# Kernel tuning notes

Measured on AMD Instinct MI355X. Metric: run time of the kernel, lower is better.

The kernel has to match this reference:

```python
import jax, jax.numpy as jnp
from jax import lax
import numpy as np

B, C, H, Wd = 32, 128, 56, 56
FILTERS = 128
KH = KW = 3
T_MIN_PREV = 0.0  # module defaults (set_params never called)
T_MIN = 0.0
T_MAX = 1.0


def setup_inputs() -> dict:
    key = jax.random.key(0)
    k1, k2 = jax.random.split(key)
    tj = jax.random.uniform(k1, (B, C, H, Wd), dtype=jnp.float32)          # spike times
    W = jax.random.normal(k2, (C * KH * KW, FILTERS), dtype=jnp.float32) * 0.02  # kernel.view(-1, filters)
    D_i = jnp.zeros((9, FILTERS), dtype=jnp.float32)                        # intrinsic delays (only row 0 used)
    return {"tj": tj, "W": W, "D_i": D_i}


def reference(tj, W, D_i):
    # 'same' padding with value t_min, then unfold + (tj - t_min) @ W is
    # exactly a zero-padded conv on (tj - t_min): the pad entries become 0.
    x = tj - T_MIN                                   # [B,C,H,W]
    # Unfold orders patch rows as (C, kh, kw); build the equivalent OIHW kernel.
    kernel = jnp.transpose(W.reshape(C, KH, KW, FILTERS), (3, 0, 1, 2))  # [F,C,KH,KW]
    y = lax.conv_general_dilated(
        x, kernel, window_strides=(1, 1), padding="SAME",
        dimension_numbers=("NCHW", "OIHW", "NCHW"))    # [B,F,H,W]
    threshold = T_MAX - T_MIN - D_i[0]                 # [F]
    ti = y + threshold[None, :, None, None] + T_MIN
    ti = jnp.minimum(ti, T_MAX)                        # torch.where(ti < t_max, ti, t_max)
    return jnp.transpose(ti, (0, 2, 3, 1))             # [B,H,W,F], matches ti.view(b,H,W,filters)
```

## Files before the change

### kernel.cpp

```cpp
#include <hip/hip_runtime.h>


#define BZ 32
#define CC 128
#define HH 56
#define WWD 56
#define HWP 3136
#define FF 128
#define PH 58
#define PW 58
#define QC 32
#define PATCH_G 2320
#define PATCH_BYTES 40960
#define BQ_OFF 81920
#define BQ_BYTES 8192
#define LDS_TOTAL 98304
#define NSTEP 36

typedef __attribute__((ext_vector_type(8))) __bf16 bf16x8;
typedef __attribute__((ext_vector_type(4))) float f32x4;
typedef __attribute__((ext_vector_type(8))) unsigned short us8;
typedef __attribute__((ext_vector_type(4))) float flt4;

__device__ __forceinline__ unsigned short f2bf(float f) {
  unsigned int u = __float_as_uint(f);
  unsigned int r = (u + 0x7FFFu + ((u >> 16) & 1u)) >> 16;
  return (unsigned short)r;
}

#define GLOAD_LDS16(g, l)                                                              \
  __builtin_amdgcn_global_load_lds((const __attribute__((address_space(1))) void*)(g), \
                                   (__attribute__((address_space(3))) void*)(l), 16, 0, 0)

__global__ void prep_w_kernel(const float* __restrict__ W, unsigned short* __restrict__ Wt) {
  int idx = blockIdx.x * 256 + threadIdx.x;
  if (idx >= 4 * 9 * 512) return;
  int qr = idx >> 9;
  int gp = idx & 511;
  int g = gp ^ ((gp >> 3) & 7);
  int q = qr / 9, r = qr - q * 9;
  int f = g >> 2, kg = g & 3;
  us8 v;
#pragma unroll
  for (int j = 0; j < 8; ++j) {
    int c = q * QC + kg * 8 + j;
    v[j] = f2bf(W[(c * 9 + r) * FF + f]);
  }
  *reinterpret_cast<us8*>(Wt + (size_t)idx * 8) = v;
}

__global__ __launch_bounds__(256) void prep_x_kernel(const float* __restrict__ x,
                                                     unsigned short* __restrict__ xp) {
  const int blk = blockIdx.x;
  const int b = blk / PH;
  const int ph = blk - b * PH;
  const int tid = threadIdx.x;
  unsigned short* dst = xp + (size_t)(b * PH + ph) * PW * CC;

  if (ph == 0 || ph == PH - 1) {
    us8 z;
#pragma unroll
    for (int k = 0; k < 8; ++k) z[k] = 0;
    for (int i = tid; i < PW * CC / 8; i += 256) reinterpret_cast<us8*>(dst)[i] = z;
    return;
  }

  __shared__ float sm[CC][57];
  const int h = ph - 1;
  {
    const int c = tid >> 1;
    const int half = tid & 1;
    const float* src = x + ((size_t)(b * CC + c)) * HWP + h * WWD + half * 28;
#pragma unroll
    for (int k = 0; k < 7; ++k) {
      flt4 v = *reinterpret_cast<const flt4*>(src + k * 4);
      sm[c][half * 28 + k * 4 + 0] = v[0];
      sm[c][half * 28 + k * 4 + 1] = v[1];
      sm[c][half * 28 + k * 4 + 2] = v[2];
      sm[c][half * 28 + k * 4 + 3] = v[3];
    }
  }
  __syncthreads();
  for (int i = tid; i < PW * 16; i += 256) {
    const int ww = i >> 4;
    const int cg = i & 15;
    us8 v;
    if (ww == 0 || ww == PW - 1) {
#pragma unroll
      for (int k = 0; k < 8; ++k) v[k] = 0;
    } else {
      const int w = ww - 1;
#pragma unroll
      for (int k = 0; k < 8; ++k) v[k] = f2bf(sm[cg * 8 + k][w]);
    }
    reinterpret_cast<us8*>(dst)[i] = v;
  }
}

struct Ctx {
  const unsigned short* xp;
  const unsigned short* Wt;
  int tid;
  int srcA[5];
  int gbase[7];
  int bOffB[4];
  f32x4 acc[7][4];
};

template <int S>
__device__ __forceinline__ void step(Ctx& c, unsigned char* lds) {
  constexpr int q = S / 9, r = S - q * 9;
  constexpr int dh = r / 3 - 1, dw = r - (r / 3) * 3 - 1;
  constexpr int tapoff = dh * 232 + dw * 4;
  constexpr bool issueA = (r < 5) && (q < 3);
  constexpr bool issueB = (S < NSTEP - 1);
  constexpr int nIssue = (issueA ? 1 : 0) + (issueB ? 1 : 0);

  if constexpr (issueA) {
    const unsigned short* src = c.xp + c.srcA[r] + (q + 1) * QC;
    unsigned char* dst = lds + ((q + 1) & 1) * PATCH_BYTES + (size_t)(r * 512 + c.tid) * 16;
    GLOAD_LDS16(src, dst);
  }
  if constexpr (issueB) {
    const unsigned short* src = c.Wt + (size_t)(S + 1) * 4096 + c.tid * 8;
    unsigned char* dst = lds + BQ_OFF + ((S + 1) & 1) * BQ_BYTES + (size_t)c.tid * 16;
    GLOAD_LDS16(src, dst);
  }
  asm volatile("s_waitcnt vmcnt(%0)" ::"n"(nIssue));
  __builtin_amdgcn_s_barrier();
  __builtin_amdgcn_sched_barrier(0);

  const unsigned char* pa = lds + (q & 1) * PATCH_BYTES;
  const unsigned char* pb = lds + BQ_OFF + (S & 1) * BQ_BYTES;
  bf16x8 af[7], bf[4];
#pragma unroll
  for (int i = 0; i < 7; ++i) {
    int g = c.gbase[i] + tapoff;
    int ga = (g ^ ((g >> 3) & 7)) << 4;
    af[i] = *reinterpret_cast<const bf16x8*>(pa + ga);
  }
#pragma unroll
  for (int j = 0; j < 4; ++j)
    bf[j] = *reinterpret_cast<const bf16x8*>(pb + c.bOffB[j]);

  __builtin_amdgcn_s_setprio(1);
#pragma unroll
  for (int i = 0; i < 7; ++i)
#pragma unroll
    for (int j = 0; j < 4; ++j)
      c.acc[i][j] = __builtin_amdgcn_mfma_f32_16x16x32_bf16(af[i], bf[j], c.acc[i][j], 0, 0, 0);
  __builtin_amdgcn_s_setprio(0);
  __builtin_amdgcn_sched_barrier(0);
  __builtin_amdgcn_s_barrier();
}

template <int S>
__device__ __forceinline__ void do_steps(Ctx& c, unsigned char* lds) {
  step<S>(c, lds);
  if constexpr (S + 1 < NSTEP) do_steps<S + 1>(c, lds);
}

__global__ __launch_bounds__(512, 2) void spiking_conv_main(
    const unsigned short* __restrict__ xp, const unsigned short* __restrict__ Wt,
    const float* __restrict__ Di, float* __restrict__ out) {
  extern __shared__ unsigned char lds[];

  const int bid = blockIdx.x;
  const int wg = (bid & 7) * 28 + (bid >> 3);
  const int b = wg / 7;
  const int ht = wg - b * 7;
  const int h0 = ht * 8;

  Ctx c;
  c.xp = xp;
  c.Wt = Wt;
  const int tid = threadIdx.x;
  c.tid = tid;
  const int lane = tid & 63, wv = tid >> 6;
  const int wr = wv >> 1, wc = wv & 1;
  const int frow = lane & 15, kg = lane >> 4;

#pragma unroll
  for (int k = 0; k < 5; ++k) {
    int gp = k * 512 + tid;
    int g = gp ^ ((gp >> 3) & 7);
    int ph = g / 232;
    int rem = g - ph * 232;
    int pw = rem >> 2;
    int kg2 = rem & 3;
    int e = ((b * PH + h0 + ph) * PW + pw) * CC + kg2 * 8;
    c.srcA[k] = (gp < PATCH_G) ? e : 0;
  }
#pragma unroll
  for (int i = 0; i < 7; ++i) {
    int t = 16 * i + frow;
    int hl = (t >= 56) ? 1 : 0;
    int wl = t - 56 * hl;
    c.gbase[i] = ((2 * wr + hl + 1) * 58 + (wl + 1)) * 4 + kg;
  }
#pragma unroll
  for (int j = 0; j < 4; ++j) {
    int gB = (wc * 64 + 16 * j + frow) * 4 + kg;
    c.bOffB[j] = (gB ^ ((gB >> 3) & 7)) << 4;
  }
  const f32x4 zero = {0.0f, 0.0f, 0.0f, 0.0f};
#pragma unroll
  for (int i = 0; i < 7; ++i)
#pragma unroll
    for (int j = 0; j < 4; ++j) c.acc[i][j] = zero;

#pragma unroll
  for (int k = 0; k < 5; ++k)
    GLOAD_LDS16(xp + c.srcA[k], lds + (size_t)(k * 512 + tid) * 16);
  GLOAD_LDS16(Wt + tid * 8, lds + BQ_OFF + (size_t)tid * 16);
  asm volatile("s_waitcnt vmcnt(0)");
  __builtin_amdgcn_s_barrier();
  __builtin_amdgcn_sched_barrier(0);

  do_steps<0>(c, lds);

#pragma unroll
  for (int j = 0; j < 4; ++j) {
    const int col = wc * 64 + 16 * j + frow;
    const float thr = 1.0f - Di[col];
#pragma unroll
    for (int i = 0; i < 7; ++i) {
      const int bt = 16 * i + kg * 4;
      const int hl = (bt >= 56) ? 1 : 0;
      const int wl0 = bt - 56 * hl;
      const int orow = h0 + 2 * wr + hl;
      const size_t obase = ((size_t)b * HWP + (size_t)orow * WWD + wl0) * FF + col;
#pragma unroll
      for (int qq = 0; qq < 4; ++qq) {
        float v = c.acc[i][j][qq] + thr;
        out[obase + (size_t)qq * FF] = fminf(v, 1.0f);
      }
    }
  }
}

__global__ __launch_bounds__(256) void spiking_conv_fallback(
    const float* __restrict__ x, const float* __restrict__ Wf,
    const float* __restrict__ Di, float* __restrict__ out) {
  __shared__ unsigned short Asm2[128][32];
  __shared__ unsigned short Bsm2[128][32];
  const int tid = threadIdx.x;
  const int m0 = blockIdx.x * 128;
  const int mi = tid & 127;
  const int half = tid >> 7;
  const int m = m0 + mi;
  const int bimg = m / HWP;
  const int p = m - bimg * HWP;
  const int h = p / WWD;
  const int w = p - h * WWD;
  const int baseA = (bimg * CC) * HWP + h * WWD + w;
  const int lane = tid & 63;
  const int wid = tid >> 6;
  const int wr = wid >> 1;
  const int wc = wid & 1;
  const int frow = lane & 15;
  const int kg = lane >> 4;
  f32x4 acc[4][4];
  const f32x4 zero = {0.0f, 0.0f, 0.0f, 0.0f};
#pragma unroll
  for (int i = 0; i < 4; ++i)
#pragma unroll
    for (int j = 0; j < 4; ++j) acc[i][j] = zero;
  for (int r = 0; r < 9; ++r) {
    const int dh = r / 3 - 1;
    const int dw = r - (r / 3) * 3 - 1;
    const int hh = h + dh;
    const int ww2 = w + dw;
    const bool valid = ((unsigned)hh < (unsigned)HH) && ((unsigned)ww2 < (unsigned)WWD);
    const int aoff2 = baseA + dh * WWD + dw + half * 16 * HWP;
    for (int c0 = 0; c0 < CC; c0 += 32) {
      __syncthreads();
      {
        const float* src = x + aoff2 + c0 * HWP;
        us8 v0, v1;
#pragma unroll
        for (int i = 0; i < 8; ++i) {
          float f0 = valid ? src[i * HWP] : 0.0f;
          float f1 = valid ? src[(i + 8) * HWP] : 0.0f;
          v0[i] = f2bf(f0);
          v1[i] = f2bf(f1);
        }
        *reinterpret_cast<us8*>(&Asm2[mi][half * 16]) = v0;
        *reinterpret_cast<us8*>(&Asm2[mi][half * 16 + 8]) = v1;
      }
      {
        us8 v0, v1;
#pragma unroll
        for (int i = 0; i < 8; ++i) {
          int cc2 = c0 + half * 16 + i;
          v0[i] = f2bf(Wf[(cc2 * 9 + r) * FF + mi]);
          v1[i] = f2bf(Wf[((cc2 + 8) * 9 + r) * FF + mi]);
        }
        *reinterpret_cast<us8*>(&Bsm2[mi][half * 16]) = v0;
        *reinterpret_cast<us8*>(&Bsm2[mi][half * 16 + 8]) = v1;
      }
      __syncthreads();
      bf16x8 af[4], bfr[4];
#pragma unroll
      for (int i = 0; i < 4; ++i)
        af[i] = *reinterpret_cast<const bf16x8*>(&Asm2[wr * 64 + i * 16 + frow][kg * 8]);
#pragma unroll
      for (int j = 0; j < 4; ++j)
        bfr[j] = *reinterpret_cast<const bf16x8*>(&Bsm2[wc * 64 + j * 16 + frow][kg * 8]);
#pragma unroll
      for (int i = 0; i < 4; ++i)
#pragma unroll
        for (int j = 0; j < 4; ++j)
          acc[i][j] = __builtin_amdgcn_mfma_f32_16x16x32_bf16(af[i], bfr[j], acc[i][j], 0, 0, 0);
    }
  }
#pragma unroll
  for (int j = 0; j < 4; ++j) {
    const int col = wc * 64 + j * 16 + frow;
    const float thr = 1.0f - Di[col];
#pragma unroll
    for (int i = 0; i < 4; ++i) {
      const int rbase = m0 + wr * 64 + i * 16 + kg * 4;
#pragma unroll
      for (int qq = 0; qq < 4; ++qq) {
        float v = acc[i][j][qq] + thr;
        out[(size_t)(rbase + qq) * FF + col] = fminf(v, 1.0f);
      }
    }
  }
}

extern "C" void kernel_launch(void* const* d_in, const int* in_sizes, int n_in,
                              void* d_out, int out_size, void* d_ws, size_t ws_size,
                              hipStream_t stream) {
  const float* tj = (const float*)d_in[0];
  const float* W = (const float*)d_in[1];
  const float* Di = (const float*)d_in[2];
  float* out = (float*)d_out;

  const size_t wt_bytes = (size_t)4 * 9 * 512 * 16;
  const size_t xp_bytes = (size_t)BZ * PH * PW * CC * 2;
  unsigned short* Wt = (unsigned short*)d_ws;
  unsigned short* xp = (unsigned short*)((char*)d_ws + wt_bytes);

  bool fast = (ws_size >= wt_bytes + xp_bytes);
  if (fast) {
    prep_w_kernel<<<72, 256, 0, stream>>>(W, Wt);
    prep_x_kernel<<<BZ * PH, 256, 0, stream>>>(tj, xp);
    spiking_conv_main<<<224, 512, LDS_TOTAL, stream>>>(xp, Wt, Di, out);
    if (hipGetLastError() != hipSuccess) fast = false;
  }
  if (!fast) {
    spiking_conv_fallback<<<100352 / 128, 256, 0, stream>>>(tj, W, Di, out);
  }
}
```

Measured before the change: 58.40 us.

## Halve conv workgroup tile, triple-buffer weights, drop LDS swizzle

The main conv kernel now runs 448 workgroups of 256 threads, each covering 4 output rows instead of 8. This gives better CU coverage on a 256-CU part and lowers LDS use per block. Weight slices are triple-buffered and prefetched two steps ahead, with a vmcnt count that tracks outstanding loads across steps, and the initial full wait is removed. The XOR swizzle on the LDS A and B layouts is dropped, which simplifies addressing but may bring back bank conflicts.

```diff
diff --git a/kernel.cpp b/kernel.cpp
--- a/kernel.cpp
+++ b/kernel.cpp
@@ -9,13 +9,12 @@
 #define FF 128
 #define PH 58
 #define PW 58
-#define QC 32
-#define PATCH_G 2320
-#define PATCH_BYTES 40960
-#define BQ_OFF 81920
-#define BQ_BYTES 8192
-#define LDS_TOTAL 98304
 #define NSTEP 36
+#define AB_BYTES 24576
+#define A_GRAN_REAL 1392
+#define BOFF 49152
+#define BB_BYTES 8192
+#define LDS_TOTAL 73728
 
 typedef __attribute__((ext_vector_type(8))) __bf16 bf16x8;
 typedef __attribute__((ext_vector_type(4))) float f32x4;
@@ -34,16 +33,15 @@
 
 __global__ void prep_w_kernel(const float* __restrict__ W, unsigned short* __restrict__ Wt) {
   int idx = blockIdx.x * 256 + threadIdx.x;
-  if (idx >= 4 * 9 * 512) return;
+  if (idx >= NSTEP * 512) return;
   int qr = idx >> 9;
-  int gp = idx & 511;
-  int g = gp ^ ((gp >> 3) & 7);
+  int g = idx & 511;
   int q = qr / 9, r = qr - q * 9;
   int f = g >> 2, kg = g & 3;
   us8 v;
 #pragma unroll
   for (int j = 0; j < 8; ++j) {
-    int c = q * QC + kg * 8 + j;
+    int c = q * 32 + kg * 8 + j;
     v[j] = f2bf(W[(c * 9 + r) * FF + f]);
   }
   *reinterpret_cast<us8*>(Wt + (size_t)idx * 8) = v;
@@ -101,7 +99,7 @@
   const unsigned short* xp;
   const unsigned short* Wt;
   int tid;
-  int srcA[5];
+  int srcA[6];
   int gbase[7];
   int bOffB[4];
   f32x4 acc[7][4];
@@ -111,34 +109,36 @@
 __device__ __forceinline__ void step(Ctx& c, unsigned char* lds) {
   constexpr int q = S / 9, r = S - q * 9;
   constexpr int dh = r / 3 - 1, dw = r - (r / 3) * 3 - 1;
-  constexpr int tapoff = dh * 232 + dw * 4;
-  constexpr bool issueA = (r < 5) && (q < 3);
-  constexpr bool issueB = (S < NSTEP - 1);
-  constexpr int nIssue = (issueA ? 1 : 0) + (issueB ? 1 : 0);
+  constexpr int tapoff = (dh * PW + dw) * 4;
+  constexpr bool issueA = (q < 3) && (r < 6);
+  constexpr bool issueB = (S <= NSTEP - 3);
+  constexpr int aS = issueA ? 1 : 0;
+  constexpr int bS = issueB ? 2 : 0;
+  constexpr int aP = (S == 0) ? 0 : ((((S - 1) / 9) < 3 && ((S - 1) % 9) < 6) ? 1 : 0);
+  constexpr int bP = (S == 0) ? 2 : (((S - 1) <= NSTEP - 3) ? 2 : 0);
+  constexpr int nOut = aS + bS + aP + bP;
 
   if constexpr (issueA) {
-    const unsigned short* src = c.xp + c.srcA[r] + (q + 1) * QC;
-    unsigned char* dst = lds + ((q + 1) & 1) * PATCH_BYTES + (size_t)(r * 512 + c.tid) * 16;
+    const unsigned short* src = c.xp + c.srcA[r] + (q + 1) * 32;
+    unsigned char* dst = lds + ((q + 1) & 1) * AB_BYTES + (size_t)(r * 256 + c.tid) * 16;
     GLOAD_LDS16(src, dst);
   }
   if constexpr (issueB) {
-    const unsigned short* src = c.Wt + (size_t)(S + 1) * 4096 + c.tid * 8;
-    unsigned char* dst = lds + BQ_OFF + ((S + 1) & 1) * BQ_BYTES + (size_t)c.tid * 16;
+    const unsigned short* src = c.Wt + (size_t)(S + 2) * 4096 + c.tid * 8;
+    unsigned char* dst = lds + BOFF + ((S + 2) % 3) * BB_BYTES + (size_t)c.tid * 16;
     GLOAD_LDS16(src, dst);
-  }
-  asm volatile("s_waitcnt vmcnt(%0)" ::"n"(nIssue));
+    GLOAD_LDS16(src + 2048, dst + 4096);
+  }
+  asm volatile("s_waitcnt vmcnt(%0)" ::"n"(nOut));
   __builtin_amdgcn_s_barrier();
   __builtin_amdgcn_sched_barrier(0);
 
-  const unsigned char* pa = lds + (q & 1) * PATCH_BYTES;
-  const unsigned char* pb = lds + BQ_OFF + (S & 1) * BQ_BYTES;
+  const unsigned char* pa = lds + (q & 1) * AB_BYTES;
+  const unsigned char* pb = lds + BOFF + (S % 3) * BB_BYTES;
   bf16x8 af[7], bf[4];
 #pragma unroll
-  for (int i = 0; i < 7; ++i) {
-    int g = c.gbase[i] + tapoff;
-    int ga = (g ^ ((g >> 3) & 7)) << 4;
-    af[i] = *reinterpret_cast<const bf16x8*>(pa + ga);
-  }
+  for (int i = 0; i < 7; ++i)
+    af[i] = *reinterpret_cast<const bf16x8*>(pa + ((c.gbase[i] + tapoff) << 4));
 #pragma unroll
   for (int j = 0; j < 4; ++j)
     bf[j] = *reinterpret_cast<const bf16x8*>(pb + c.bOffB[j]);
@@ -160,16 +160,16 @@
   if constexpr (S + 1 < NSTEP) do_steps<S + 1>(c, lds);
 }
 
-__global__ __launch_bounds__(512, 2) void spiking_conv_main(
+__global__ __launch_bounds__(256, 2) void spiking_conv_main(
     const unsigned short* __restrict__ xp, const unsigned short* __restrict__ Wt,
     const float* __restrict__ Di, float* __restrict__ out) {
   extern __shared__ unsigned char lds[];
 
   const int bid = blockIdx.x;
-  const int wg = (bid & 7) * 28 + (bid >> 3);
-  const int b = wg / 7;
-  const int ht = wg - b * 7;
-  const int h0 = ht * 8;
+  const int wg = (bid & 7) * 56 + (bid >> 3);
+  const int b = wg / 14;
+  const int rg = wg - b * 14;
+  const int h0 = rg * 4;
 
   Ctx c;
   c.xp = xp;
@@ -181,28 +181,26 @@
   const int frow = lane & 15, kg = lane >> 4;
 
 #pragma unroll
-  for (int k = 0; k < 5; ++k) {
-    int gp = k * 512 + tid;
-    int g = gp ^ ((gp >> 3) & 7);
-    int ph = g / 232;
-    int rem = g - ph * 232;
-    int pw = rem >> 2;
+  for (int k = 0; k < 6; ++k) {
+    int g = k * 256 + tid;
+    if (g >= A_GRAN_REAL) g = 0;
+    int prow = g / 232;
+    int rem = g - prow * 232;
+    int px = rem >> 2;
     int kg2 = rem & 3;
-    int e = ((b * PH + h0 + ph) * PW + pw) * CC + kg2 * 8;
-    c.srcA[k] = (gp < PATCH_G) ? e : 0;
+    c.srcA[k] = ((b * PH + h0 + prow) * PW + px) * CC + kg2 * 8;
   }
 #pragma unroll
   for (int i = 0; i < 7; ++i) {
     int t = 16 * i + frow;
-    int hl = (t >= 56) ? 1 : 0;
-    int wl = t - 56 * hl;
-    c.gbase[i] = ((2 * wr + hl + 1) * 58 + (wl + 1)) * 4 + kg;
-  }
-#pragma unroll
-  for (int j = 0; j < 4; ++j) {
-    int gB = (wc * 64 + 16 * j + frow) * 4 + kg;
-    c.bOffB[j] = (gB ^ ((gB >> 3) & 7)) << 4;
-  }
+    int rowb = (t >= 56) ? 1 : 0;
+    int col = t - 56 * rowb;
+    c.gbase[i] = ((2 * wr + rowb + 1) * PW + (col + 1)) * 4 + kg;
+  }
+#pragma unroll
+  for (int j = 0; j < 4; ++j)
+    c.bOffB[j] = ((wc * 64 + 16 * j + frow) * 4 + kg) << 4;
+
   const f32x4 zero = {0.0f, 0.0f, 0.0f, 0.0f};
 #pragma unroll
   for (int i = 0; i < 7; ++i)
@@ -210,12 +208,12 @@
     for (int j = 0; j < 4; ++j) c.acc[i][j] = zero;
 
 #pragma unroll
-  for (int k = 0; k < 5; ++k)
-    GLOAD_LDS16(xp + c.srcA[k], lds + (size_t)(k * 512 + tid) * 16);
-  GLOAD_LDS16(Wt + tid * 8, lds + BQ_OFF + (size_t)tid * 16);
-  asm volatile("s_waitcnt vmcnt(0)");
-  __builtin_amdgcn_s_barrier();
-  __builtin_amdgcn_sched_barrier(0);
+  for (int k = 0; k < 6; ++k)
+    GLOAD_LDS16(xp + c.srcA[k], lds + (size_t)(k * 256 + tid) * 16);
+  GLOAD_LDS16(Wt + tid * 8, lds + BOFF + (size_t)tid * 16);
+  GLOAD_LDS16(Wt + 2048 + tid * 8, lds + BOFF + 4096 + (size_t)tid * 16);
+  GLOAD_LDS16(Wt + 4096 + tid * 8, lds + BOFF + BB_BYTES + (size_t)tid * 16);
+  GLOAD_LDS16(Wt + 6144 + tid * 8, lds + BOFF + BB_BYTES + 4096 + (size_t)tid * 16);
 
   do_steps<0>(c, lds);
 
@@ -226,9 +224,9 @@
 #pragma unroll
     for (int i = 0; i < 7; ++i) {
       const int bt = 16 * i + kg * 4;
-      const int hl = (bt >= 56) ? 1 : 0;
-      const int wl0 = bt - 56 * hl;
-      const int orow = h0 + 2 * wr + hl;
+      const int rowb = (bt >= 56) ? 1 : 0;
+      const int wl0 = bt - 56 * rowb;
+      const int orow = h0 + 2 * wr + rowb;
       const size_t obase = ((size_t)b * HWP + (size_t)orow * WWD + wl0) * FF + col;
 #pragma unroll
       for (int qq = 0; qq < 4; ++qq) {
@@ -338,7 +336,7 @@
   const float* Di = (const float*)d_in[2];
   float* out = (float*)d_out;
 
-  const size_t wt_bytes = (size_t)4 * 9 * 512 * 16;
+  const size_t wt_bytes = (size_t)NSTEP * 512 * 16;
   const size_t xp_bytes = (size_t)BZ * PH * PW * CC * 2;
   unsigned short* Wt = (unsigned short*)d_ws;
   unsigned short* xp = (unsigned short*)((char*)d_ws + wt_bytes);
@@ -347,7 +345,7 @@
   if (fast) {
     prep_w_kernel<<<72, 256, 0, stream>>>(W, Wt);
     prep_x_kernel<<<BZ * PH, 256, 0, stream>>>(tj, xp);
-    spiking_conv_main<<<224, 512, LDS_TOTAL, stream>>>(xp, Wt, Di, out);
+    spiking_conv_main<<<448, 256, LDS_TOTAL, stream>>>(xp, Wt, Di, out);
     if (hipGetLastError() != hipSuccess) fast = false;
   }
   if (!fast) {
```

Result: faster. 53.48 us (-8.4%).
